# Performance work log

Measured on AMD Instinct MI355X. Metric: run time of the kernel, lower is better.

The kernel has to match this reference:

```python
import jax, jax.numpy as jnp
import numpy as np

DIM, HEADS, MLP_HID = 1024, 16, 4096
B, N = 2, 2048
EPS = 1e-5

def setup_inputs() -> dict:
    key = jax.random.key(0)
    ks = jax.random.split(key, 8)
    s = lambda fan_in: 1.0 / np.sqrt(fan_in)
    return {
        "x": jax.random.normal(ks[0], (B, N, DIM), jnp.float32),
        "ln1_w": jnp.ones((DIM,), jnp.float32),
        "ln1_b": jnp.zeros((DIM,), jnp.float32),
        # weights stored [in, out] (transpose of torch Linear.weight)
        "qkv_w": jax.random.normal(ks[1], (DIM, 3 * DIM), jnp.float32) * s(DIM),
        "proj_w": jax.random.normal(ks[2], (DIM, DIM), jnp.float32) * s(DIM),
        "proj_b": jnp.zeros((DIM,), jnp.float32),
        "ln2_w": jnp.ones((DIM,), jnp.float32),
        "ln2_b": jnp.zeros((DIM,), jnp.float32),
        "fc1_w": jax.random.normal(ks[3], (DIM, MLP_HID), jnp.float32) * s(DIM),
        "fc1_b": jnp.zeros((MLP_HID,), jnp.float32),
        "fc2_w": jax.random.normal(ks[4], (MLP_HID, DIM), jnp.float32) * s(MLP_HID),
        "fc2_b": jnp.zeros((DIM,), jnp.float32),
    }

def _layernorm(x, w, b):
    mu = jnp.mean(x, axis=-1, keepdims=True)
    var = jnp.mean(jnp.square(x - mu), axis=-1, keepdims=True)
    return (x - mu) * jax.lax.rsqrt(var + EPS) * w + b

def reference(x, ln1_w, ln1_b, qkv_w, proj_w, proj_b, ln2_w, ln2_b, fc1_w, fc1_b, fc2_w, fc2_b):
    Bn, Nn, C = x.shape
    H, D = HEADS, C // HEADS
    scale = D ** -0.5

    # --- attention sub-block (pre-norm, residual) ---
    h = _layernorm(x, ln1_w, ln1_b)
    qkv = (h @ qkv_w).reshape(Bn, Nn, 3, H, D)
    q, k, v = jnp.moveaxis(qkv, 2, 0)  # each [B, N, H, D]
    attn = jnp.einsum('bnhd,bmhd->bhnm', q, k) * scale
    attn = jax.nn.softmax(attn, axis=-1)
    o = jnp.einsum('bhnm,bmhd->bnhd', attn, v).reshape(Bn, Nn, C)
    x = x + (o @ proj_w + proj_b)

    # --- MLP sub-block (pre-norm, residual) ---
    h = _layernorm(x, ln2_w, ln2_b)
    h = jax.nn.gelu(h @ fc1_w + fc1_b, approximate=False)
    x = x + (h @ fc2_w + fc2_b)
    return x
```

## Files before the change

kernel.cpp:

```cpp
#include <hip/hip_runtime.h>
#include <hip/hip_bf16.h>

typedef __attribute__((ext_vector_type(4))) float  f32x4;
typedef __attribute__((ext_vector_type(8))) short  short8;
typedef __attribute__((ext_vector_type(8))) unsigned short ushort8;
typedef __attribute__((ext_vector_type(4))) unsigned short u16x4;
typedef unsigned short u16;

__device__ __forceinline__ u16 f2bf(float f) {
    unsigned int u = __builtin_bit_cast(unsigned int, f);
    return (u16)((u + 0x7fffu + ((u >> 16) & 1u)) >> 16);
}

__device__ __forceinline__ f32x4 mfma16(short8 a, short8 b, f32x4 c) {
    return __builtin_amdgcn_mfma_f32_16x16x32_bf16(a, b, c, 0, 0, 0);
}

__device__ __forceinline__ float fexp2(float x) {
    float r;
    asm("v_exp_f32 %0, %1" : "=v"(r) : "v"(x));
    return r;
}

__device__ __forceinline__ float fgelu(float v) {
    const float t = v * v;
    const float u = v * (-2.302118f - 0.102944f * t);
    return v / (1.0f + fexp2(u));
}

__device__ __forceinline__ void gload_lds16(const u16* g, u16* l) {
    __builtin_amdgcn_global_load_lds(
        (__attribute__((address_space(1))) void*)(uintptr_t)(g),
        (__attribute__((address_space(3))) void*)(unsigned)(uintptr_t)(l),
        16, 0, 0);
}

__device__ __forceinline__ void BAR() {
    __builtin_amdgcn_sched_barrier(0);
    __builtin_amdgcn_s_barrier();
    __builtin_amdgcn_sched_barrier(0);
}

__global__ __launch_bounds__(256) void tcast_kernel(const float* __restrict__ W,
                                                    u16* __restrict__ Wt,
                                                    int K, int N) {
    __shared__ float tile[32][33];
    const int tx = threadIdx.x & 31, ty = threadIdx.x >> 5;
    const int c0 = blockIdx.x * 32;
    const int r0 = blockIdx.y * 32;
#pragma unroll
    for (int i = 0; i < 32; i += 8)
        tile[ty + i][tx] = W[(size_t)(r0 + ty + i) * N + c0 + tx];
    __syncthreads();
#pragma unroll
    for (int i = 0; i < 32; i += 8)
        Wt[(size_t)(c0 + ty + i) * K + r0 + tx] = f2bf(tile[tx][ty + i]);
}

__global__ __launch_bounds__(256) void ln_kernel(const float* __restrict__ x,
                                                 const float* __restrict__ w,
                                                 const float* __restrict__ b,
                                                 u16* __restrict__ out) {
    const int row = blockIdx.x;
    const int tid = threadIdx.x;
    const float4 v = ((const float4*)(x + (size_t)row * 1024))[tid];
    float s1 = v.x + v.y + v.z + v.w;
    float s2 = v.x * v.x + v.y * v.y + v.z * v.z + v.w * v.w;
#pragma unroll
    for (int m = 1; m < 64; m <<= 1) { s1 += __shfl_xor(s1, m); s2 += __shfl_xor(s2, m); }
    __shared__ float red1[4], red2[4];
    const int wave = tid >> 6, lane = tid & 63;
    if (lane == 0) { red1[wave] = s1; red2[wave] = s2; }
    __syncthreads();
    s1 = red1[0] + red1[1] + red1[2] + red1[3];
    s2 = red2[0] + red2[1] + red2[2] + red2[3];
    const float mean = s1 * (1.0f / 1024.0f);
    const float var  = s2 * (1.0f / 1024.0f) - mean * mean;
    const float rstd = rsqrtf(var + 1e-5f);
    const float4 wv = ((const float4*)w)[tid];
    const float4 bv = ((const float4*)b)[tid];
    u16x4 o;
    o[0] = f2bf((v.x - mean) * rstd * wv.x + bv.x);
    o[1] = f2bf((v.y - mean) * rstd * wv.y + bv.y);
    o[2] = f2bf((v.z - mean) * rstd * wv.z + bv.z);
    o[3] = f2bf((v.w - mean) * rstd * wv.w + bv.w);
    *(u16x4*)(out + (size_t)row * 1024 + tid * 4) = o;
}

template <int BN, int HAS_BIAS, int HAS_RES, int DO_GELU, int OUT_BF16>
__global__ __launch_bounds__(512, 2) void gemm8_kernel(const u16* __restrict__ A,
                                                       const u16* __restrict__ Bt,
                                                       const float* __restrict__ bias,
                                                       const float* __restrict__ res,
                                                       void* __restrict__ Cout,
                                                       int M, int N, int K) {
    constexpr int NTN = BN / 64;
    constexpr int BH  = BN / 2;
    constexpr int BSW = BH / 64;
    __shared__ __align__(16) u16 Asl[2][2][128 * 64];
    __shared__ __align__(16) u16 Bsl[2][2][BH * 64];
    const int tid = threadIdx.x;
    const int wave = tid >> 6, lane = tid & 63;
    const int wr = wave >> 2, wc = wave & 3;
    const int fq = lane >> 4, fr = lane & 15;
    const size_t bm = (size_t)blockIdx.y * 256, bn = (size_t)blockIdx.x * BN;
    const int hb = wc >> 1;
    const int brow0 = (wc & 1) * (BN / 4);

    const int rx = fr & 7;
    const int ko0 = ((0 + fq) ^ rx) * 8;
    const int ko1 = ((4 + fq) ^ rx) * 8;

    f32x4 acc[8][NTN] = {};

    auto STAGE = [&](int buf, int k0) {
#pragma unroll
        for (int h = 0; h < 2; h++)
#pragma unroll
            for (int s = 0; s < 2; s++) {
                const int task = tid + s * 512;
                const int row = task >> 3, seg2 = (task & 7) ^ (row & 7);
                gload_lds16(A + (bm + h * 128 + row) * (size_t)K + k0 + seg2 * 8,
                            &Asl[buf][h][(wave * 64 + s * 512) * 8]);
            }
#pragma unroll
        for (int h = 0; h < 2; h++)
#pragma unroll
            for (int s = 0; s < BSW; s++) {
                const int task = tid + s * 512;
                const int row = task >> 3, seg2 = (task & 7) ^ (row & 7);
                gload_lds16(Bt + (bn + h * BH + row) * (size_t)K + k0 + seg2 * 8,
                            &Bsl[buf][h][(wave * 64 + s * 512) * 8]);
            }
    };

    STAGE(0, 0);
    asm volatile("s_waitcnt vmcnt(0)" ::: "memory");
    __builtin_amdgcn_s_barrier();
    int cur = 0;

    for (int k0 = 0; k0 < K; k0 += 64) {
        short8 bfr[NTN][2];
#pragma unroll
        for (int q = 0; q < 4; q++) {
            if (q == 0) {
#pragma unroll
                for (int nt = 0; nt < NTN; nt++) {
                    const int r16 = brow0 + nt * 16 + fr;
                    bfr[nt][0] = *(const short8*)&Bsl[cur][hb][r16 * 64 + ko0];
                    bfr[nt][1] = *(const short8*)&Bsl[cur][hb][r16 * 64 + ko1];
                }
            }
            short8 afr[2][2];
#pragma unroll
            for (int m2 = 0; m2 < 2; m2++) {
                const int r16 = (q * 2 + m2) * 16 + fr;
                afr[m2][0] = *(const short8*)&Asl[cur][wr][r16 * 64 + ko0];
                afr[m2][1] = *(const short8*)&Asl[cur][wr][r16 * 64 + ko1];
            }
            if (q == 0 && k0 + 64 < K) STAGE(cur ^ 1, k0 + 64);
            BAR();
            __builtin_amdgcn_s_setprio(1);
#pragma unroll
            for (int ksu = 0; ksu < 2; ksu++)
#pragma unroll
                for (int m2 = 0; m2 < 2; m2++)
#pragma unroll
                    for (int nt = 0; nt < NTN; nt++)
                        acc[q * 2 + m2][nt] = mfma16(afr[m2][ksu], bfr[nt][ksu],
                                                     acc[q * 2 + m2][nt]);
            __builtin_amdgcn_s_setprio(0);
            if (q == 3) {
                asm volatile("s_waitcnt vmcnt(0)" ::: "memory");
            }
            BAR();
        }
        cur ^= 1;
    }
#pragma unroll
    for (int mt = 0; mt < 8; mt++) {
#pragma unroll
        for (int nt = 0; nt < NTN; nt++) {
            const size_t col = bn + wc * (BN / 4) + nt * 16 + fr;
            const float bb = HAS_BIAS ? bias[col] : 0.0f;
#pragma unroll
            for (int j = 0; j < 4; j++) {
                const size_t row = bm + wr * 128 + mt * 16 + fq * 4 + j;
                float v = acc[mt][nt][j] + bb;
                if (DO_GELU) v = fgelu(v);
                if (HAS_RES) v += res[row * N + col];
                if (OUT_BF16) ((u16*)Cout)[row * N + col] = f2bf(v);
                else          ((float*)Cout)[row * N + col] = v;
            }
        }
    }
}

template <int HAS_BIAS, int HAS_RES, int DO_GELU, int OUT_BF16>
__global__ __launch_bounds__(256) void gemm_kernel(const u16* __restrict__ A,
                                                   const u16* __restrict__ Bt,
                                                   const float* __restrict__ bias,
                                                   const float* __restrict__ res,
                                                   void* __restrict__ Cout,
                                                   int M, int N, int K) {
    __shared__ __align__(16) u16 As[2][128 * 64];
    __shared__ __align__(16) u16 Bs[2][128 * 64];
    const int tid = threadIdx.x;
    const int wave = tid >> 6, lane = tid & 63;
    const int wr = wave >> 1, wc = wave & 1;
    const int fq = lane >> 4, fr = lane & 15;
    const size_t bm = (size_t)blockIdx.y * 128, bn = (size_t)blockIdx.x * 128;
    const int lr = lane >> 3, seg = lane & 7;
    const int seg2 = seg ^ (lr & 7);

    const u16* Ab = A  + bm * (size_t)K + seg2 * 8;
    const u16* Bb = Bt + bn * (size_t)K + seg2 * 8;

    const int rx = fr & 7;
    const int ko0 = ((0 + fq) ^ rx) * 8;
    const int ko1 = ((4 + fq) ^ rx) * 8;

    f32x4 acc[4][4] = {};

    auto STAGE = [&](int buf, int k0) {
#pragma unroll
        for (int i = 0; i < 4; i++) {
            const int r = wave * 32 + i * 8 + lr;
            gload_lds16(Ab + (size_t)r * K + k0, &As[buf][(wave * 4 + i) * 512]);
            gload_lds16(Bb + (size_t)r * K + k0, &Bs[buf][(wave * 4 + i) * 512]);
        }
    };

    STAGE(0, 0);
    __syncthreads();
    int cur = 0;

    for (int k0 = 0; k0 < K; k0 += 64) {
        if (k0 + 64 < K) STAGE(cur ^ 1, k0 + 64);
#pragma unroll
        for (int ks = 0; ks < 2; ks++) {
            const int ko = ks ? ko1 : ko0;
            short8 af[4], bf[4];
#pragma unroll
            for (int t = 0; t < 4; t++) {
                af[t] = *(const short8*)&As[cur][(wr * 64 + t * 16 + fr) * 64 + ko];
                bf[t] = *(const short8*)&Bs[cur][(wc * 64 + t * 16 + fr) * 64 + ko];
            }
#pragma unroll
            for (int mt = 0; mt < 4; mt++)
#pragma unroll
                for (int nt = 0; nt < 4; nt++)
                    acc[mt][nt] = mfma16(af[mt], bf[nt], acc[mt][nt]);
        }
        __syncthreads();
        cur ^= 1;
    }
#pragma unroll
    for (int mt = 0; mt < 4; mt++) {
#pragma unroll
        for (int nt = 0; nt < 4; nt++) {
            const size_t col = bn + wc * 64 + nt * 16 + fr;
            const float bb = HAS_BIAS ? bias[col] : 0.0f;
#pragma unroll
            for (int j = 0; j < 4; j++) {
                const size_t row = bm + wr * 64 + mt * 16 + fq * 4 + j;
                float v = acc[mt][nt][j] + bb;
                if (DO_GELU) v = fgelu(v);
                if (HAS_RES) v += res[row * N + col];
                if (OUT_BF16) ((u16*)Cout)[row * N + col] = f2bf(v);
                else          ((float*)Cout)[row * N + col] = v;
            }
        }
    }
}

__global__ __launch_bounds__(512) void attn_kernel(const u16* __restrict__ qkv,
                                                   u16* __restrict__ O) {
    const int bh = blockIdx.x;
    const int b = bh >> 4, h = bh & 15;
    const int qb = blockIdx.y;
    const int tid = threadIdx.x, wave = tid >> 6, lane = tid & 63;
    const int fq = lane >> 4, fr = lane & 15;
    __shared__ __align__(16) u16 Ks[2][64 * 72];
    __shared__ __align__(16) u16 Vt[2][64 * 72];
    __shared__ __align__(16) u16 Pl[8][16 * 72];

    const size_t base = (size_t)b * 2048 * 3072;
    const int q0 = qb * 128 + wave * 16;

    short8 qf[2];
#pragma unroll
    for (int ks = 0; ks < 2; ks++)
        qf[ks] = *(const short8*)(qkv + base + (size_t)(q0 + fr) * 3072 + h * 64 + ks * 32 + fq * 8);

    const u16* kp = qkv + base + 1024 + (size_t)h * 64;
    const u16* vp = qkv + base + 2048 + (size_t)h * 64;
    const int krow = tid >> 3, kseg = tid & 7;
    const int vkey = tid & 63, vdc = tid >> 6;

    f32x4 accO[4] = {};
    float mq = -1e30f, lq = 0.0f;

    const float c = 0.125f * 1.44269504f;

    ushort8 kreg = *(const ushort8*)(kp + (size_t)krow * 3072 + kseg * 8);
    ushort8 vreg = *(const ushort8*)(vp + (size_t)vkey * 3072 + vdc * 8);
    *(ushort8*)&Ks[0][krow * 72 + kseg * 8] = kreg;
#pragma unroll
    for (int j = 0; j < 8; j++) Vt[0][(vdc * 8 + j) * 72 + vkey] = vreg[j];
    __syncthreads();
    int cur = 0;

    for (int kt = 0; kt < 32; kt++) {
        if (kt < 31) {
            kreg = *(const ushort8*)(kp + (size_t)((kt + 1) * 64 + krow) * 3072 + kseg * 8);
            vreg = *(const ushort8*)(vp + (size_t)((kt + 1) * 64 + vkey) * 3072 + vdc * 8);
        }
        f32x4 s[4];
#pragma unroll
        for (int nt = 0; nt < 4; nt++) {
            f32x4 a = {};
#pragma unroll
            for (int ks = 0; ks < 2; ks++) {
                short8 kf = *(const short8*)&Ks[cur][(nt * 16 + fr) * 72 + ks * 32 + fq * 8];
                a = mfma16(kf, qf[ks], a);
            }
#pragma unroll
            for (int j = 0; j < 4; j++) s[nt][j] = a[j] * c;
        }
        float pm = -1e30f;
#pragma unroll
        for (int nt = 0; nt < 4; nt++) {
            const float m01 = fmaxf(s[nt][0], s[nt][1]);
            const float m23 = fmaxf(s[nt][2], s[nt][3]);
            pm = fmaxf(pm, fmaxf(m01, m23));
        }
        pm = fmaxf(pm, __shfl_xor(pm, 16));
        pm = fmaxf(pm, __shfl_xor(pm, 32));
        const float mn = fmaxf(mq, pm);
        const float aq = fexp2(mq - mn);
        mq = mn;
        float lsum = 0.0f;
#pragma unroll
        for (int nt = 0; nt < 4; nt++)
#pragma unroll
            for (int j = 0; j < 4; j++) {
                const float pij = fexp2(s[nt][j] - mn);
                s[nt][j] = pij;
                lsum += pij;
            }
        lsum += __shfl_xor(lsum, 16);
        lsum += __shfl_xor(lsum, 32);
        lq = lq * aq + lsum;
        float ar[4];
#pragma unroll
        for (int j = 0; j < 4; j++) ar[j] = __shfl(aq, fq * 4 + j);
#pragma unroll
        for (int dt = 0; dt < 4; dt++)
#pragma unroll
            for (int j = 0; j < 4; j++) accO[dt][j] *= ar[j];
#pragma unroll
        for (int nt = 0; nt < 4; nt++)
#pragma unroll
            for (int j = 0; j < 4; j++)
                Pl[wave][fr * 72 + nt * 16 + fq * 4 + j] = f2bf(s[nt][j]);
#pragma unroll
        for (int ks = 0; ks < 2; ks++) {
            short8 pf = *(const short8*)&Pl[wave][fr * 72 + ks * 32 + fq * 8];
#pragma unroll
            for (int dt = 0; dt < 4; dt++) {
                short8 vf = *(const short8*)&Vt[cur][(dt * 16 + fr) * 72 + ks * 32 + fq * 8];
                accO[dt] = mfma16(pf, vf, accO[dt]);
            }
        }
        if (kt < 31) {
            *(ushort8*)&Ks[cur ^ 1][krow * 72 + kseg * 8] = kreg;
#pragma unroll
            for (int j = 0; j < 8; j++) Vt[cur ^ 1][(vdc * 8 + j) * 72 + vkey] = vreg[j];
        }
        __syncthreads();
        cur ^= 1;
    }
    float rq[4];
#pragma unroll
    for (int j = 0; j < 4; j++) rq[j] = 1.0f / __shfl(lq, fq * 4 + j);
#pragma unroll
    for (int dt = 0; dt < 4; dt++)
#pragma unroll
        for (int j = 0; j < 4; j++) {
            const float v = accO[dt][j] * rq[j];
            O[(size_t)(b * 2048 + q0 + fq * 4 + j) * 1024 + h * 64 + dt * 16 + fr] = f2bf(v);
        }
}

extern "C" void kernel_launch(void* const* d_in, const int* in_sizes, int n_in,
                              void* d_out, int out_size, void* d_ws, size_t ws_size,
                              hipStream_t stream) {
    (void)in_sizes; (void)n_in; (void)out_size; (void)ws_size;
    const float* x     = (const float*)d_in[0];
    const float* ln1w  = (const float*)d_in[1];
    const float* ln1b  = (const float*)d_in[2];
    const float* qkvw  = (const float*)d_in[3];
    const float* projw = (const float*)d_in[4];
    const float* projb = (const float*)d_in[5];
    const float* ln2w  = (const float*)d_in[6];
    const float* ln2b  = (const float*)d_in[7];
    const float* fc1w  = (const float*)d_in[8];
    const float* fc1b  = (const float*)d_in[9];
    const float* fc2w  = (const float*)d_in[10];
    const float* fc2b  = (const float*)d_in[11];

    char* p = (char*)d_ws;
    auto alloc = [&](size_t bytes) { void* r = p; p += (bytes + 255) & ~(size_t)255; return r; };
    u16* wt_qkv  = (u16*)alloc(3072ull * 1024 * 2);
    u16* wt_proj = (u16*)alloc(1024ull * 1024 * 2);
    u16* wt_fc1  = (u16*)alloc(4096ull * 1024 * 2);
    u16* wt_fc2  = (u16*)alloc(1024ull * 4096 * 2);
    u16* h1      = (u16*)alloc(4096ull * 1024 * 2);
    u16* qkv     = (u16*)alloc(4096ull * 3072 * 2);
    u16* attn_o  = (u16*)alloc(4096ull * 1024 * 2);
    u16* h2      = (u16*)alloc(4096ull * 1024 * 2);
    u16* mlp_h   = (u16*)alloc(4096ull * 4096 * 2);
    float* x1 = (float*)d_out;

    tcast_kernel<<<dim3(96, 32),  256, 0, stream>>>(qkvw,  wt_qkv, 1024, 3072);
    tcast_kernel<<<dim3(32, 32),  256, 0, stream>>>(projw, wt_proj, 1024, 1024);
    tcast_kernel<<<dim3(128, 32), 256, 0, stream>>>(fc1w,  wt_fc1, 1024, 4096);
    tcast_kernel<<<dim3(32, 128), 256, 0, stream>>>(fc2w,  wt_fc2, 4096, 1024);

    ln_kernel<<<4096, 256, 0, stream>>>(x, ln1w, ln1b, h1);
    gemm8_kernel<256, 0, 0, 0, 1><<<dim3(12, 16), 512, 0, stream>>>(h1, wt_qkv, nullptr, nullptr, qkv, 4096, 3072, 1024);
    attn_kernel<<<dim3(32, 16), 512, 0, stream>>>(qkv, attn_o);
    gemm_kernel<1, 1, 0, 0><<<dim3(8, 32), 256, 0, stream>>>(attn_o, wt_proj, projb, x, x1, 4096, 1024, 1024);

    ln_kernel<<<4096, 256, 0, stream>>>(x1, ln2w, ln2b, h2);
    gemm8_kernel<256, 1, 0, 1, 1><<<dim3(16, 16), 512, 0, stream>>>(h2, wt_fc1, fc1b, nullptr, mlp_h, 4096, 4096, 1024);
    gemm_kernel<1, 1, 0, 0><<<dim3(8, 32), 256, 0, stream>>>(mlp_h, wt_fc2, fc2b, x1, d_out, 4096, 1024, 4096);
}
```

Before: 253.5 us.

## Swizzle attention LDS layout and route proj/fc2 GEMMs through gemm8 kernel

The attention kernel drops its padded 72-wide LDS rows for 64-wide rows with an XOR swizzle on K, V^T and P tiles. It also writes P as 4-wide vector stores. This is meant to avoid bank conflicts while using less shared memory. The proj and fc2 GEMMs now use the 8-wave gemm8 kernel with a 256x128 tile instead of the 128x128 gemm_kernel, which is removed. That halves the grid to 128 blocks, which may underfill the GPU's compute units.

After: 275.8 us. 1.09x slower.

```diff
diff --git a/kernel.cpp b/kernel.cpp
--- a/kernel.cpp
+++ b/kernel.cpp
@@ -196,84 +196,6 @@
     }
 }
 
-template <int HAS_BIAS, int HAS_RES, int DO_GELU, int OUT_BF16>
-__global__ __launch_bounds__(256) void gemm_kernel(const u16* __restrict__ A,
-                                                   const u16* __restrict__ Bt,
-                                                   const float* __restrict__ bias,
-                                                   const float* __restrict__ res,
-                                                   void* __restrict__ Cout,
-                                                   int M, int N, int K) {
-    __shared__ __align__(16) u16 As[2][128 * 64];
-    __shared__ __align__(16) u16 Bs[2][128 * 64];
-    const int tid = threadIdx.x;
-    const int wave = tid >> 6, lane = tid & 63;
-    const int wr = wave >> 1, wc = wave & 1;
-    const int fq = lane >> 4, fr = lane & 15;
-    const size_t bm = (size_t)blockIdx.y * 128, bn = (size_t)blockIdx.x * 128;
-    const int lr = lane >> 3, seg = lane & 7;
-    const int seg2 = seg ^ (lr & 7);
-
-    const u16* Ab = A  + bm * (size_t)K + seg2 * 8;
-    const u16* Bb = Bt + bn * (size_t)K + seg2 * 8;
-
-    const int rx = fr & 7;
-    const int ko0 = ((0 + fq) ^ rx) * 8;
-    const int ko1 = ((4 + fq) ^ rx) * 8;
-
-    f32x4 acc[4][4] = {};
-
-    auto STAGE = [&](int buf, int k0) {
-#pragma unroll
-        for (int i = 0; i < 4; i++) {
-            const int r = wave * 32 + i * 8 + lr;
-            gload_lds16(Ab + (size_t)r * K + k0, &As[buf][(wave * 4 + i) * 512]);
-            gload_lds16(Bb + (size_t)r * K + k0, &Bs[buf][(wave * 4 + i) * 512]);
-        }
-    };
-
-    STAGE(0, 0);
-    __syncthreads();
-    int cur = 0;
-
-    for (int k0 = 0; k0 < K; k0 += 64) {
-        if (k0 + 64 < K) STAGE(cur ^ 1, k0 + 64);
-#pragma unroll
-        for (int ks = 0; ks < 2; ks++) {
-            const int ko = ks ? ko1 : ko0;
-            short8 af[4], bf[4];
-#pragma unroll
-            for (int t = 0; t < 4; t++) {
-                af[t] = *(const short8*)&As[cur][(wr * 64 + t * 16 + fr) * 64 + ko];
-                bf[t] = *(const short8*)&Bs[cur][(wc * 64 + t * 16 + fr) * 64 + ko];
-            }
-#pragma unroll
-            for (int mt = 0; mt < 4; mt++)
-#pragma unroll
-                for (int nt = 0; nt < 4; nt++)
-                    acc[mt][nt] = mfma16(af[mt], bf[nt], acc[mt][nt]);
-        }
-        __syncthreads();
-        cur ^= 1;
-    }
-#pragma unroll
-    for (int mt = 0; mt < 4; mt++) {
-#pragma unroll
-        for (int nt = 0; nt < 4; nt++) {
-            const size_t col = bn + wc * 64 + nt * 16 + fr;
-            const float bb = HAS_BIAS ? bias[col] : 0.0f;
-#pragma unroll
-            for (int j = 0; j < 4; j++) {
-                const size_t row = bm + wr * 64 + mt * 16 + fq * 4 + j;
-                float v = acc[mt][nt][j] + bb;
-                if (DO_GELU) v = fgelu(v);
-                if (HAS_RES) v += res[row * N + col];
-                if (OUT_BF16) ((u16*)Cout)[row * N + col] = f2bf(v);
-                else          ((float*)Cout)[row * N + col] = v;
-            }
-        }
-    }
-}
-
 __global__ __launch_bounds__(512) void attn_kernel(const u16* __restrict__ qkv,
                                                    u16* __restrict__ O) {
     const int bh = blockIdx.x;
@@ -281,9 +203,9 @@
     const int qb = blockIdx.y;
     const int tid = threadIdx.x, wave = tid >> 6, lane = tid & 63;
     const int fq = lane >> 4, fr = lane & 15;
-    __shared__ __align__(16) u16 Ks[2][64 * 72];
-    __shared__ __align__(16) u16 Vt[2][64 * 72];
-    __shared__ __align__(16) u16 Pl[8][16 * 72];
+    __shared__ __align__(16) u16 Ks[2][64 * 64];
+    __shared__ __align__(16) u16 Vt[2][64 * 64];
+    __shared__ __align__(16) u16 Pl[8][16 * 64];
 
     const size_t base = (size_t)b * 2048 * 3072;
     const int q0 = qb * 128 + wave * 16;
@@ -296,7 +218,12 @@
     const u16* kp = qkv + base + 1024 + (size_t)h * 64;
     const u16* vp = qkv + base + 2048 + (size_t)h * 64;
     const int krow = tid >> 3, kseg = tid & 7;
+    const int kpos = (kseg ^ (krow & 7)) * 8;
     const int vkey = tid & 63, vdc = tid >> 6;
+
+    const int rx = fr & 7;
+    const int ko0 = ((0 + fq) ^ rx) * 8;
+    const int ko1 = ((4 + fq) ^ rx) * 8;
 
     f32x4 accO[4] = {};
     float mq = -1e30f, lq = 0.0f;
@@ -305,9 +232,12 @@
 
     ushort8 kreg = *(const ushort8*)(kp + (size_t)krow * 3072 + kseg * 8);
     ushort8 vreg = *(const ushort8*)(vp + (size_t)vkey * 3072 + vdc * 8);
-    *(ushort8*)&Ks[0][krow * 72 + kseg * 8] = kreg;
-#pragma unroll
-    for (int j = 0; j < 8; j++) Vt[0][(vdc * 8 + j) * 72 + vkey] = vreg[j];
+    *(ushort8*)&Ks[0][krow * 64 + kpos] = kreg;
+#pragma unroll
+    for (int j = 0; j < 8; j++) {
+        const int row = vdc * 8 + j;
+        Vt[0][row * 64 + ((vkey >> 3) ^ (row & 7)) * 8 + (vkey & 7)] = vreg[j];
+    }
     __syncthreads();
     int cur = 0;
 
@@ -320,11 +250,10 @@
 #pragma unroll
         for (int nt = 0; nt < 4; nt++) {
             f32x4 a = {};
-#pragma unroll
-            for (int ks = 0; ks < 2; ks++) {
-                short8 kf = *(const short8*)&Ks[cur][(nt * 16 + fr) * 72 + ks * 32 + fq * 8];
-                a = mfma16(kf, qf[ks], a);
-            }
+            short8 kf0 = *(const short8*)&Ks[cur][(nt * 16 + fr) * 64 + ko0];
+            short8 kf1 = *(const short8*)&Ks[cur][(nt * 16 + fr) * 64 + ko1];
+            a = mfma16(kf0, qf[0], a);
+            a = mfma16(kf1, qf[1], a);
 #pragma unroll
             for (int j = 0; j < 4; j++) s[nt][j] = a[j] * c;
         }
@@ -360,23 +289,30 @@
 #pragma unroll
             for (int j = 0; j < 4; j++) accO[dt][j] *= ar[j];
 #pragma unroll
-        for (int nt = 0; nt < 4; nt++)
-#pragma unroll
-            for (int j = 0; j < 4; j++)
-                Pl[wave][fr * 72 + nt * 16 + fq * 4 + j] = f2bf(s[nt][j]);
+        for (int nt = 0; nt < 4; nt++) {
+            u16x4 pw;
+#pragma unroll
+            for (int j = 0; j < 4; j++) pw[j] = f2bf(s[nt][j]);
+            const int chunk = nt * 2 + (fq >> 1);
+            *(u16x4*)&Pl[wave][fr * 64 + (chunk ^ rx) * 8 + (fq & 1) * 4] = pw;
+        }
 #pragma unroll
         for (int ks = 0; ks < 2; ks++) {
-            short8 pf = *(const short8*)&Pl[wave][fr * 72 + ks * 32 + fq * 8];
+            const int ko = ks ? ko1 : ko0;
+            short8 pf = *(const short8*)&Pl[wave][fr * 64 + ko];
 #pragma unroll
             for (int dt = 0; dt < 4; dt++) {
-                short8 vf = *(const short8*)&Vt[cur][(dt * 16 + fr) * 72 + ks * 32 + fq * 8];
+                short8 vf = *(const short8*)&Vt[cur][(dt * 16 + fr) * 64 + ko];
                 accO[dt] = mfma16(pf, vf, accO[dt]);
             }
         }
         if (kt < 31) {
-            *(ushort8*)&Ks[cur ^ 1][krow * 72 + kseg * 8] = kreg;
-#pragma unroll
-            for (int j = 0; j < 8; j++) Vt[cur ^ 1][(vdc * 8 + j) * 72 + vkey] = vreg[j];
+            *(ushort8*)&Ks[cur ^ 1][krow * 64 + kpos] = kreg;
+#pragma unroll
+            for (int j = 0; j < 8; j++) {
+                const int row = vdc * 8 + j;
+                Vt[cur ^ 1][row * 64 + ((vkey >> 3) ^ (row & 7)) * 8 + (vkey & 7)] = vreg[j];
+            }
         }
         __syncthreads();
         cur ^= 1;
@@ -431,9 +367,9 @@
     ln_kernel<<<4096, 256, 0, stream>>>(x, ln1w, ln1b, h1);
     gemm8_kernel<256, 0, 0, 0, 1><<<dim3(12, 16), 512, 0, stream>>>(h1, wt_qkv, nullptr, nullptr, qkv, 4096, 3072, 1024);
     attn_kernel<<<dim3(32, 16), 512, 0, stream>>>(qkv, attn_o);
-    gemm_kernel<1, 1, 0, 0><<<dim3(8, 32), 256, 0, stream>>>(attn_o, wt_proj, projb, x, x1, 4096, 1024, 1024);
+    gemm8_kernel<128, 1, 1, 0, 0><<<dim3(8, 16), 512, 0, stream>>>(attn_o, wt_proj, projb, x, x1, 4096, 1024, 1024);
 
     ln_kernel<<<4096, 256, 0, stream>>>(x1, ln2w, ln2b, h2);
     gemm8_kernel<256, 1, 0, 1, 1><<<dim3(16, 16), 512, 0, stream>>>(h2, wt_fc1, fc1b, nullptr, mlp_h, 4096, 4096, 1024);
-    gemm_kernel<1, 1, 0, 0><<<dim3(8, 32), 256, 0, stream>>>(mlp_h, wt_fc2, fc2b, x1, d_out, 4096, 1024, 4096);
-}
+    gemm8_kernel<128, 1, 1, 0, 0><<<dim3(8, 16), 512, 0, stream>>>(mlp_h, wt_fc2, fc2b, x1, d_out, 4096, 1024, 4096);
+}
```
